# Performance work log

Hardware: AMD Instinct MI355X
Metric: run time of the kernel (lower is better)

The kernel has to match this reference:

```python
import jax, jax.numpy as jnp
import numpy as np

B = 4096
SEQ = 128            # window_size * rnn_in_pkts
WINDOW = 32
IN_PKTS = 4
LEN_V, LEN_E = 1500, 64
IPD_V, IPD_E = 256, 64
EV = 64              # embedding_vector_bits
RNN_IN = IN_PKTS * EV   # 256
H = 256              # rnn_hidden_bits
LABELS = 100


def setup_inputs() -> dict:
    key = jax.random.key(0)
    ks = jax.random.split(key, 12)
    s = 0.05
    return {
        "len_x": jax.random.randint(ks[0], (B, SEQ), 0, LEN_V),
        "ipd_x": jax.random.randint(ks[1], (B, SEQ), 0, IPD_V),
        "len_emb": jax.random.normal(ks[2], (LEN_V, LEN_E), jnp.float32) * s,
        "ipd_emb": jax.random.normal(ks[3], (IPD_V, IPD_E), jnp.float32) * s,
        "fc_w": jax.random.normal(ks[4], (EV, LEN_E + IPD_E), jnp.float32) * s,
        "fc_b": jax.random.normal(ks[5], (EV,), jnp.float32) * s,
        "w_ih": jax.random.normal(ks[6], (3 * H, RNN_IN), jnp.float32) * s,
        "w_hh": jax.random.normal(ks[7], (3 * H, H), jnp.float32) * s,
        "b_ih": jax.random.normal(ks[8], (3 * H,), jnp.float32) * s,
        "b_hh": jax.random.normal(ks[9], (3 * H,), jnp.float32) * s,
        "out_w": jax.random.normal(ks[10], (LABELS, H), jnp.float32) * s,
        "out_b": jax.random.normal(ks[11], (LABELS,), jnp.float32) * s,
    }


def _gru_scan(rnn_in, w_ih, w_hh, b_ih, b_hh):
    # rnn_in: [B, T, RNN_IN]. Precompute input-side gates for all steps at once.
    gi_all = jnp.einsum("bti,gi->btg", rnn_in, w_ih) + b_ih  # [B,T,3H]
    h0 = jnp.zeros((rnn_in.shape[0], H), rnn_in.dtype)

    def step(h, gi):
        gh = h @ w_hh.T + b_hh                 # [B,3H]
        i_r, i_z, i_n = jnp.split(gi, 3, axis=-1)
        h_r, h_z, h_n = jnp.split(gh, 3, axis=-1)
        r = jax.nn.sigmoid(i_r + h_r)
        z = jax.nn.sigmoid(i_z + h_z)
        n = jnp.tanh(i_n + r * h_n)
        h_new = (1.0 - z) * n + z * h
        return h_new, None

    h_final, _ = jax.lax.scan(step, h0, jnp.swapaxes(gi_all, 0, 1))
    return h_final


def reference(len_x, ipd_x, len_emb, ipd_emb, fc_w, fc_b, w_ih, w_hh, b_ih, b_hh, out_w, out_b):
    len_e = len_emb[len_x]                      # [B,SEQ,LEN_E]
    ipd_e = ipd_emb[ipd_x]                      # [B,SEQ,IPD_E]
    cat = jnp.concatenate([len_e, ipd_e], axis=-1)
    evs = cat @ fc_w.T + fc_b                   # [B,SEQ,EV]
    rnn_in = evs.reshape(B, WINDOW, RNN_IN)     # [B,32,256]
    h = _gru_scan(rnn_in, w_ih, w_hh, b_ih, b_hh)
    logits = h @ out_w.T + out_b                # [B,LABELS]
    return logits
```

## Files before the change

kernel.cpp:

```cpp
#include <hip/hip_runtime.h>
#include <hip/hip_bf16.h>

typedef __bf16 bf16_t;
typedef __bf16 bf16x8 __attribute__((ext_vector_type(8)));
typedef float f32x4 __attribute__((ext_vector_type(4)));
typedef unsigned short u16x4 __attribute__((ext_vector_type(4)));

#define MFMA16(a, b, c) __builtin_amdgcn_mfma_f32_16x16x32_bf16((a), (b), (c), 0, 0, 0)

#define BATCH 4096
#define SEQN 128
#define HN 256
#define NLABELS 100
#define TSTEPS 32
#define LEN_VN 1500
#define IPD_VN 256

#define OFF_LENT   0u
#define OFF_IPDT   384000u
#define OFF_WIH    449536u
#define OFF_WHH    842752u
#define OFF_GI     1235968u

__device__ __forceinline__ float sigf(float x) {
    return __builtin_amdgcn_rcpf(1.f + __expf(-x));
}
__device__ __forceinline__ float tanh_fast(float x) {
    return 2.f * __builtin_amdgcn_rcpf(1.f + __expf(-2.f * x)) - 1.f;
}
__device__ __forceinline__ float b2f(unsigned short v) {
    union { unsigned u; float f; } c; c.u = ((unsigned)v) << 16; return c.f;
}
__device__ __forceinline__ f32x4 b2f4(u16x4 v) {
    f32x4 o;
    #pragma unroll
    for (int r = 0; r < 4; ++r) o[r] = b2f(v[r]);
    return o;
}
__device__ __forceinline__ unsigned short f2b(float f) {
    union { bf16_t h; unsigned short s; } c; c.h = (bf16_t)f; return c.s;
}

__device__ __forceinline__ void barrier_lds() {
    asm volatile("s_waitcnt lgkmcnt(0)\n\ts_barrier" ::: "memory");
}

__global__ void prep_kernel(const float* __restrict__ len_emb,
                            const float* __restrict__ ipd_emb,
                            const float* __restrict__ fc_w,
                            const float* __restrict__ fc_b,
                            const float* __restrict__ w_ih,
                            const float* __restrict__ w_hh,
                            float* __restrict__ lenT, float* __restrict__ ipdT,
                            bf16_t* __restrict__ wfrag_ih,
                            bf16_t* __restrict__ wfrag_hh) {
    const int bid = blockIdx.x, tid = threadIdx.x;
    if (bid < 439) {
        const int row = bid * 4 + (tid >> 6);
        const int e = tid & 63;
        if (row < LEN_VN) {
            const float* emb = len_emb + row * 64;
            const float* wv = fc_w + e * 128;
            float s = fc_b[e];
            #pragma unroll 8
            for (int j = 0; j < 64; ++j) s += emb[j] * wv[j];
            lenT[row * 64 + e] = s;
        } else if (row < LEN_VN + IPD_VN) {
            const int v = row - LEN_VN;
            const float* emb = ipd_emb + v * 64;
            const float* wv = fc_w + e * 128 + 64;
            float s = 0.f;
            #pragma unroll 8
            for (int j = 0; j < 64; ++j) s += emb[j] * wv[j];
            ipdT[v * 64 + e] = s;
        }
    } else {
        const int flat = (bid - 439) * 256 + tid;
        const int which = flat / 24576;
        const int rem = flat % 24576;
        const int c = rem >> 9;
        const int kt = (rem >> 6) & 7;
        const int lane = rem & 63;
        const int g = c * 16 + (lane & 15);
        const int k0 = kt * 32 + (lane >> 4) * 8;
        const float* src = (which == 0 ? w_ih : w_hh) + g * 256 + k0;
        bf16_t* dst = (which == 0 ? wfrag_ih : wfrag_hh) + ((c * 8 + kt) * 64 + lane) * 8;
        f32x4 s0 = *(const f32x4*)(src);
        f32x4 s1 = *(const f32x4*)(src + 4);
        bf16x8 o;
        #pragma unroll
        for (int j = 0; j < 4; ++j) { o[j] = (bf16_t)s0[j]; o[4 + j] = (bf16_t)s1[j]; }
        *(bf16x8*)dst = o;
    }
}

__global__ void __launch_bounds__(512, 2)
gemm_gi(const int* __restrict__ len_x, const int* __restrict__ ipd_x,
        const float* __restrict__ lenT, const float* __restrict__ ipdT,
        const bf16_t* __restrict__ wfrag_ih,
        const float* __restrict__ b_ih, const float* __restrict__ b_hh,
        bf16_t* __restrict__ gi) {
    __shared__ bf16_t wlds[8 * 8 * 512];
    __shared__ bf16_t a_lds[2][8 * 512];

    const int tid = threadIdx.x;
    const int lane = tid & 63;
    const int w = tid >> 6;
    const int bt = blockIdx.x;
    const int quad = lane >> 4;

    const int cts[6] = {2*w, 2*w + 1, 16 + 2*w, 17 + 2*w, 32 + 2*w, 33 + 2*w};

    bf16x8 wr[5][8];
    #pragma unroll
    for (int cc = 0; cc < 5; ++cc)
        #pragma unroll
        for (int kt = 0; kt < 8; ++kt)
            wr[cc][kt] = *(const bf16x8*)(wfrag_ih + ((cts[cc] * 8 + kt) * 64 + lane) * 8);
    #pragma unroll
    for (int kt = 0; kt < 8; ++kt)
        *(bf16x8*)&wlds[(w * 8 + kt) * 512 + lane * 8] =
            *(const bf16x8*)(wfrag_ih + ((cts[5] * 8 + kt) * 64 + lane) * 8);

    f32x4 bias[6];
    #pragma unroll
    for (int cc = 0; cc < 6; ++cc) {
        f32x4 v = *(const f32x4*)(b_ih + cts[cc] * 16 + quad * 4);
        if (cc < 4) v += *(const f32x4*)(b_hh + cts[cc] * 16 + quad * 4);
        bias[cc] = v;
    }

    const int pair = tid >> 3;
    const int sub = tid & 7;
    const int grow = pair & 15;
    const int p = pair >> 4;
    const int e0 = sub * 8;
    const int b_row = bt * 16 + grow;
    const int goff = (2 * p + (sub >> 2)) * 512 + ((sub & 3) * 16 + grow) * 8;

    auto do_gather = [&](int t) {
        const int seq = t * 4 + p;
        const int v1 = len_x[b_row * SEQN + seq];
        const int v2 = ipd_x[b_row * SEQN + seq];
        const float* lp = lenT + v1 * 64 + e0;
        const float* ip = ipdT + v2 * 64 + e0;
        f32x4 a0 = *(const f32x4*)lp + *(const f32x4*)ip;
        f32x4 a1 = *(const f32x4*)(lp + 4) + *(const f32x4*)(ip + 4);
        bf16x8 o;
        #pragma unroll
        for (int j = 0; j < 4; ++j) { o[j] = (bf16_t)a0[j]; o[4 + j] = (bf16_t)a1[j]; }
        *(bf16x8*)&a_lds[t & 1][goff] = o;
    };

    do_gather(0);
    bf16_t* gib = gi + (size_t)bt * 48 * 32 * 256 + lane * 4;
    const bf16_t* wb = &wlds[w * 8 * 512 + lane * 8];

    for (int t = 0; t < TSTEPS; ++t) {
        barrier_lds();
        if (t + 1 < TSTEPS) do_gather(t + 1);

        f32x4 acc[6];
        #pragma unroll
        for (int cc = 0; cc < 6; ++cc) acc[cc] = bias[cc];

        const bf16_t* ab = &a_lds[t & 1][lane * 8];
        #pragma unroll
        for (int kt = 0; kt < 8; ++kt) {
            bf16x8 xf = *(const bf16x8*)(ab + kt * 512);
            bf16x8 w5 = *(const bf16x8*)(wb + kt * 512);
            acc[0] = MFMA16(wr[0][kt], xf, acc[0]);
            acc[1] = MFMA16(wr[1][kt], xf, acc[1]);
            acc[2] = MFMA16(wr[2][kt], xf, acc[2]);
            acc[3] = MFMA16(wr[3][kt], xf, acc[3]);
            acc[4] = MFMA16(wr[4][kt], xf, acc[4]);
            acc[5] = MFMA16(w5, xf, acc[5]);
        }

        #pragma unroll
        for (int cc = 0; cc < 6; ++cc) {
            u16x4 o;
            #pragma unroll
            for (int r = 0; r < 4; ++r) o[r] = f2b(acc[cc][r]);
            *(u16x4*)(gib + ((size_t)cts[cc] * 32 + t) * 256) = o;
        }
    }
}

__global__ void __launch_bounds__(1024, 4)
gru_kernel(const bf16_t* __restrict__ gi,
           const bf16_t* __restrict__ wfrag_hh,
           const float* __restrict__ b_hh,
           const float* __restrict__ out_w,
           const float* __restrict__ out_b,
           float* __restrict__ out) {
    __shared__ char smem[147456];
    bf16_t* wlds = (bf16_t*)smem;
    bf16_t* h_lds = (bf16_t*)(smem + 131072);
    float* h_fin = (float*)smem;

    const int tid = threadIdx.x;
    const int lane = tid & 63;
    const int w = tid >> 6;
    const int bt = blockIdx.x;
    const int quad = lane >> 4;
    const int b = lane & 15;

    bf16x8 wr[2][8];
    #pragma unroll
    for (int cc = 0; cc < 2; ++cc) {
        const int ct = cc * 16 + w;
        #pragma unroll
        for (int kt = 0; kt < 8; ++kt)
            wr[cc][kt] = *(const bf16x8*)(wfrag_hh + ((ct * 8 + kt) * 64 + lane) * 8);
    }
    #pragma unroll
    for (int kt = 0; kt < 8; ++kt)
        *(bf16x8*)&wlds[(w * 8 + kt) * 512 + lane * 8] =
            *(const bf16x8*)(wfrag_hh + (((32 + w) * 8 + kt) * 64 + lane) * 8);

    const f32x4 bhn = *(const f32x4*)(b_hh + (32 + w) * 16 + quad * 4);

    for (int i = tid; i < 4096; i += 1024) h_lds[4096 + i] = (bf16_t)0.f;

    const int j0 = 16 * w + 4 * quad;
    const int woff = (j0 >> 5) * 512 + ((((j0 >> 3) & 3)) * 16 + b) * 8 + (j0 & 7);

    const bf16_t* gib = gi + (size_t)bt * 48 * 32 * 256 + lane * 4;
    const bf16_t* wb = &wlds[w * 8 * 512 + lane * 8];

    u16x4 gc0 = *(const u16x4*)(gib + ((size_t)(w) * 32) * 256);
    u16x4 gc1 = *(const u16x4*)(gib + ((size_t)(16 + w) * 32) * 256);
    u16x4 gc2 = *(const u16x4*)(gib + ((size_t)(32 + w) * 32) * 256);

    f32x4 hprev = {};

    for (int t = 0; t < TSTEPS; ++t) {
        barrier_lds();

        f32x4 acc0 = b2f4(gc0);
        f32x4 acc1 = b2f4(gc1);
        f32x4 acc2 = bhn;
        u16x4 g2cur = gc2;

        if (t + 1 < TSTEPS) {
            gc0 = *(const u16x4*)(gib + ((size_t)(w) * 32 + t + 1) * 256);
            gc1 = *(const u16x4*)(gib + ((size_t)(16 + w) * 32 + t + 1) * 256);
            gc2 = *(const u16x4*)(gib + ((size_t)(32 + w) * 32 + t + 1) * 256);
        }

        const bf16_t* hb = &h_lds[((t + 1) & 1) * 4096 + lane * 8];
        #pragma unroll
        for (int kt = 0; kt < 8; ++kt) {
            bf16x8 hf = *(const bf16x8*)(hb + kt * 512);
            bf16x8 w5 = *(const bf16x8*)(wb + kt * 512);
            acc0 = MFMA16(wr[0][kt], hf, acc0);
            acc1 = MFMA16(wr[1][kt], hf, acc1);
            acc2 = MFMA16(w5, hf, acc2);
        }

        f32x4 rg, zg;
        #pragma unroll
        for (int r = 0; r < 4; ++r) { rg[r] = sigf(acc0[r]); zg[r] = sigf(acc1[r]); }
        f32x4 u = b2f4(g2cur) + rg * acc2;
        f32x4 ng;
        #pragma unroll
        for (int r = 0; r < 4; ++r) ng[r] = tanh_fast(u[r]);
        f32x4 hn = ng + zg * (hprev - ng);
        hprev = hn;

        u16x4 o;
        #pragma unroll
        for (int r = 0; r < 4; ++r) o[r] = f2b(hn[r]);
        *(u16x4*)(&h_lds[(t & 1) * 4096 + woff]) = o;
    }

    __syncthreads();

    *(f32x4*)(h_fin + b * 260 + j0) = hprev;
    __syncthreads();

    for (int i = tid; i < 16 * NLABELS; i += 1024) {
        const int row = i / NLABELS;
        const int cl = i - row * NLABELS;
        const f32x4* wrow = (const f32x4*)(out_w + cl * 256);
        const f32x4* hr = (const f32x4*)(h_fin + row * 260);
        f32x4 acc = {0.f, 0.f, 0.f, 0.f};
        #pragma unroll 4
        for (int k = 0; k < 64; ++k) acc += hr[k] * wrow[k];
        out[(bt * 16 + row) * NLABELS + cl] =
            out_b[cl] + acc[0] + acc[1] + acc[2] + acc[3];
    }
}

extern "C" void kernel_launch(void* const* d_in, const int* in_sizes, int n_in,
                              void* d_out, int out_size, void* d_ws, size_t ws_size,
                              hipStream_t stream) {
    (void)in_sizes; (void)n_in; (void)out_size; (void)ws_size;
    const int*   len_x   = (const int*)d_in[0];
    const int*   ipd_x   = (const int*)d_in[1];
    const float* len_emb = (const float*)d_in[2];
    const float* ipd_emb = (const float*)d_in[3];
    const float* fc_w    = (const float*)d_in[4];
    const float* fc_b    = (const float*)d_in[5];
    const float* w_ih    = (const float*)d_in[6];
    const float* w_hh    = (const float*)d_in[7];
    const float* b_ih    = (const float*)d_in[8];
    const float* b_hh    = (const float*)d_in[9];
    const float* out_w   = (const float*)d_in[10];
    const float* out_b   = (const float*)d_in[11];

    char* ws = (char*)d_ws;
    float*  lenT = (float*)(ws + OFF_LENT);
    float*  ipdT = (float*)(ws + OFF_IPDT);
    bf16_t* wfi  = (bf16_t*)(ws + OFF_WIH);
    bf16_t* wfh  = (bf16_t*)(ws + OFF_WHH);
    bf16_t* gi   = (bf16_t*)(ws + OFF_GI);

    prep_kernel<<<631, 256, 0, stream>>>(len_emb, ipd_emb, fc_w, fc_b,
                                         w_ih, w_hh, lenT, ipdT, wfi, wfh);
    gemm_gi<<<256, 512, 0, stream>>>(len_x, ipd_x, lenT, ipdT, wfi,
                                     b_ih, b_hh, gi);
    gru_kernel<<<256, 1024, 0, stream>>>(gi, wfh, b_hh, out_w, out_b,
                                         (float*)d_out);
}
```

Baseline: 234.4 us.

## Fuse input-gate GEMM into GRU kernel, dropping separate gemm_gi launch

Merges the input-projection GEMM that produced gi into the GRU recurrence kernel. Each 1024-thread block first computes its own batch tile's input gates for all timesteps, with 16 waves each covering three column tiles and half the threads doing the embedding gather. It writes them to global memory, waits on vmcnt, then runs the recurrence reading them back. This removes a kernel launch and lets each block's gi data stay hot in cache, at the cost of less parallelism per block during the GEMM phase and an extra full-block sync.

```diff
diff --git a/kernel.cpp b/kernel.cpp
--- a/kernel.cpp
+++ b/kernel.cpp
@@ -43,6 +43,9 @@
 
 __device__ __forceinline__ void barrier_lds() {
     asm volatile("s_waitcnt lgkmcnt(0)\n\ts_barrier" ::: "memory");
+}
+__device__ __forceinline__ void wait_vm0() {
+    asm volatile("s_waitcnt vmcnt(0)" ::: "memory");
 }
 
 __global__ void prep_kernel(const float* __restrict__ len_emb,
@@ -94,109 +97,19 @@
     }
 }
 
-__global__ void __launch_bounds__(512, 2)
-gemm_gi(const int* __restrict__ len_x, const int* __restrict__ ipd_x,
-        const float* __restrict__ lenT, const float* __restrict__ ipdT,
-        const bf16_t* __restrict__ wfrag_ih,
-        const float* __restrict__ b_ih, const float* __restrict__ b_hh,
-        bf16_t* __restrict__ gi) {
-    __shared__ bf16_t wlds[8 * 8 * 512];
-    __shared__ bf16_t a_lds[2][8 * 512];
-
-    const int tid = threadIdx.x;
-    const int lane = tid & 63;
-    const int w = tid >> 6;
-    const int bt = blockIdx.x;
-    const int quad = lane >> 4;
-
-    const int cts[6] = {2*w, 2*w + 1, 16 + 2*w, 17 + 2*w, 32 + 2*w, 33 + 2*w};
-
-    bf16x8 wr[5][8];
-    #pragma unroll
-    for (int cc = 0; cc < 5; ++cc)
-        #pragma unroll
-        for (int kt = 0; kt < 8; ++kt)
-            wr[cc][kt] = *(const bf16x8*)(wfrag_ih + ((cts[cc] * 8 + kt) * 64 + lane) * 8);
-    #pragma unroll
-    for (int kt = 0; kt < 8; ++kt)
-        *(bf16x8*)&wlds[(w * 8 + kt) * 512 + lane * 8] =
-            *(const bf16x8*)(wfrag_ih + ((cts[5] * 8 + kt) * 64 + lane) * 8);
-
-    f32x4 bias[6];
-    #pragma unroll
-    for (int cc = 0; cc < 6; ++cc) {
-        f32x4 v = *(const f32x4*)(b_ih + cts[cc] * 16 + quad * 4);
-        if (cc < 4) v += *(const f32x4*)(b_hh + cts[cc] * 16 + quad * 4);
-        bias[cc] = v;
-    }
-
-    const int pair = tid >> 3;
-    const int sub = tid & 7;
-    const int grow = pair & 15;
-    const int p = pair >> 4;
-    const int e0 = sub * 8;
-    const int b_row = bt * 16 + grow;
-    const int goff = (2 * p + (sub >> 2)) * 512 + ((sub & 3) * 16 + grow) * 8;
-
-    auto do_gather = [&](int t) {
-        const int seq = t * 4 + p;
-        const int v1 = len_x[b_row * SEQN + seq];
-        const int v2 = ipd_x[b_row * SEQN + seq];
-        const float* lp = lenT + v1 * 64 + e0;
-        const float* ip = ipdT + v2 * 64 + e0;
-        f32x4 a0 = *(const f32x4*)lp + *(const f32x4*)ip;
-        f32x4 a1 = *(const f32x4*)(lp + 4) + *(const f32x4*)(ip + 4);
-        bf16x8 o;
-        #pragma unroll
-        for (int j = 0; j < 4; ++j) { o[j] = (bf16_t)a0[j]; o[4 + j] = (bf16_t)a1[j]; }
-        *(bf16x8*)&a_lds[t & 1][goff] = o;
-    };
-
-    do_gather(0);
-    bf16_t* gib = gi + (size_t)bt * 48 * 32 * 256 + lane * 4;
-    const bf16_t* wb = &wlds[w * 8 * 512 + lane * 8];
-
-    for (int t = 0; t < TSTEPS; ++t) {
-        barrier_lds();
-        if (t + 1 < TSTEPS) do_gather(t + 1);
-
-        f32x4 acc[6];
-        #pragma unroll
-        for (int cc = 0; cc < 6; ++cc) acc[cc] = bias[cc];
-
-        const bf16_t* ab = &a_lds[t & 1][lane * 8];
-        #pragma unroll
-        for (int kt = 0; kt < 8; ++kt) {
-            bf16x8 xf = *(const bf16x8*)(ab + kt * 512);
-            bf16x8 w5 = *(const bf16x8*)(wb + kt * 512);
-            acc[0] = MFMA16(wr[0][kt], xf, acc[0]);
-            acc[1] = MFMA16(wr[1][kt], xf, acc[1]);
-            acc[2] = MFMA16(wr[2][kt], xf, acc[2]);
-            acc[3] = MFMA16(wr[3][kt], xf, acc[3]);
-            acc[4] = MFMA16(wr[4][kt], xf, acc[4]);
-            acc[5] = MFMA16(w5, xf, acc[5]);
-        }
-
-        #pragma unroll
-        for (int cc = 0; cc < 6; ++cc) {
-            u16x4 o;
-            #pragma unroll
-            for (int r = 0; r < 4; ++r) o[r] = f2b(acc[cc][r]);
-            *(u16x4*)(gib + ((size_t)cts[cc] * 32 + t) * 256) = o;
-        }
-    }
-}
-
 __global__ void __launch_bounds__(1024, 4)
-gru_kernel(const bf16_t* __restrict__ gi,
-           const bf16_t* __restrict__ wfrag_hh,
-           const float* __restrict__ b_hh,
-           const float* __restrict__ out_w,
-           const float* __restrict__ out_b,
-           float* __restrict__ out) {
+fused_kernel(const int* __restrict__ len_x, const int* __restrict__ ipd_x,
+             const float* __restrict__ lenT, const float* __restrict__ ipdT,
+             const bf16_t* __restrict__ wfrag_ih,
+             const bf16_t* __restrict__ wfrag_hh,
+             const float* __restrict__ b_ih, const float* __restrict__ b_hh,
+             bf16_t* gi,
+             const float* __restrict__ out_w,
+             const float* __restrict__ out_b,
+             float* __restrict__ out) {
     __shared__ char smem[147456];
     bf16_t* wlds = (bf16_t*)smem;
-    bf16_t* h_lds = (bf16_t*)(smem + 131072);
+    bf16_t* dbuf = (bf16_t*)(smem + 131072);
     float* h_fin = (float*)smem;
 
     const int tid = threadIdx.x;
@@ -206,6 +119,85 @@
     const int quad = lane >> 4;
     const int b = lane & 15;
 
+    bf16_t* gib = gi + (size_t)bt * 48 * 32 * 256 + lane * 4;
+    const bf16_t* wb = &wlds[w * 8 * 512 + lane * 8];
+
+    {
+        bf16x8 wri[2][8];
+        #pragma unroll
+        for (int cc = 0; cc < 2; ++cc) {
+            const int ct = cc * 16 + w;
+            #pragma unroll
+            for (int kt = 0; kt < 8; ++kt)
+                wri[cc][kt] = *(const bf16x8*)(wfrag_ih + ((ct * 8 + kt) * 64 + lane) * 8);
+        }
+        #pragma unroll
+        for (int kt = 0; kt < 8; ++kt)
+            *(bf16x8*)&wlds[(w * 8 + kt) * 512 + lane * 8] =
+                *(const bf16x8*)(wfrag_ih + (((32 + w) * 8 + kt) * 64 + lane) * 8);
+
+        f32x4 bias0 = *(const f32x4*)(b_ih + w * 16 + quad * 4)
+                    + *(const f32x4*)(b_hh + w * 16 + quad * 4);
+        f32x4 bias1 = *(const f32x4*)(b_ih + 256 + w * 16 + quad * 4)
+                    + *(const f32x4*)(b_hh + 256 + w * 16 + quad * 4);
+        f32x4 bias2 = *(const f32x4*)(b_ih + 512 + w * 16 + quad * 4);
+
+        const int sub = tid & 511;
+        const int pr = sub >> 3;
+        const int sub8 = sub & 7;
+        const int grow = pr & 15;
+        const int p = pr >> 4;
+        const int e0 = sub8 * 8;
+        const int b_row = bt * 16 + grow;
+        const int goff = (2 * p + (sub8 >> 2)) * 512 + ((sub8 & 3) * 16 + grow) * 8;
+
+        auto do_gather = [&](int t) {
+            const int seq = t * 4 + p;
+            const int v1 = len_x[b_row * SEQN + seq];
+            const int v2 = ipd_x[b_row * SEQN + seq];
+            const float* lp = lenT + v1 * 64 + e0;
+            const float* ip = ipdT + v2 * 64 + e0;
+            f32x4 a0 = *(const f32x4*)lp + *(const f32x4*)ip;
+            f32x4 a1 = *(const f32x4*)(lp + 4) + *(const f32x4*)(ip + 4);
+            bf16x8 o;
+            #pragma unroll
+            for (int j = 0; j < 4; ++j) { o[j] = (bf16_t)a0[j]; o[4 + j] = (bf16_t)a1[j]; }
+            *(bf16x8*)&dbuf[(t & 1) * 4096 + goff] = o;
+        };
+
+        if (tid < 512) do_gather(0);
+
+        for (int t = 0; t < TSTEPS; ++t) {
+            barrier_lds();
+            if (t + 1 < TSTEPS && tid < 512) do_gather(t + 1);
+
+            f32x4 acc0 = bias0, acc1 = bias1, acc2 = bias2;
+            const bf16_t* ab = &dbuf[(t & 1) * 4096 + lane * 8];
+            #pragma unroll
+            for (int kt = 0; kt < 8; ++kt) {
+                bf16x8 xf = *(const bf16x8*)(ab + kt * 512);
+                bf16x8 w5 = *(const bf16x8*)(wb + kt * 512);
+                acc0 = MFMA16(wri[0][kt], xf, acc0);
+                acc1 = MFMA16(wri[1][kt], xf, acc1);
+                acc2 = MFMA16(w5, xf, acc2);
+            }
+
+            u16x4 o0, o1, o2;
+            #pragma unroll
+            for (int r = 0; r < 4; ++r) {
+                o0[r] = f2b(acc0[r]); o1[r] = f2b(acc1[r]); o2[r] = f2b(acc2[r]);
+            }
+            *(u16x4*)(gib + ((size_t)(w) * 32 + t) * 256) = o0;
+            *(u16x4*)(gib + ((size_t)(16 + w) * 32 + t) * 256) = o1;
+            *(u16x4*)(gib + ((size_t)(32 + w) * 32 + t) * 256) = o2;
+        }
+    }
+
+    barrier_lds();
+    wait_vm0();
+
+    bf16_t* h_lds = dbuf;
+
     bf16x8 wr[2][8];
     #pragma unroll
     for (int cc = 0; cc < 2; ++cc) {
@@ -225,9 +217,6 @@
 
     const int j0 = 16 * w + 4 * quad;
     const int woff = (j0 >> 5) * 512 + ((((j0 >> 3) & 3)) * 16 + b) * 8 + (j0 & 7);
-
-    const bf16_t* gib = gi + (size_t)bt * 48 * 32 * 256 + lane * 4;
-    const bf16_t* wb = &wlds[w * 8 * 512 + lane * 8];
 
     u16x4 gc0 = *(const u16x4*)(gib + ((size_t)(w) * 32) * 256);
     u16x4 gc1 = *(const u16x4*)(gib + ((size_t)(16 + w) * 32) * 256);
@@ -319,8 +308,7 @@
 
     prep_kernel<<<631, 256, 0, stream>>>(len_emb, ipd_emb, fc_w, fc_b,
                                          w_ih, w_hh, lenT, ipdT, wfi, wfh);
-    gemm_gi<<<256, 512, 0, stream>>>(len_x, ipd_x, lenT, ipdT, wfi,
-                                     b_ih, b_hh, gi);
-    gru_kernel<<<256, 1024, 0, stream>>>(gi, wfh, b_hh, out_w, out_b,
-                                         (float*)d_out);
-}
+    fused_kernel<<<256, 1024, 0, stream>>>(len_x, ipd_x, lenT, ipdT, wfi, wfh,
+                                           b_ih, b_hh, gi, out_w, out_b,
+                                           (float*)d_out);
+}
```

Result: no change. 232.6 us (-0.8%).
